# Kernel optimization log

Hardware: AMD Instinct MI355X
Metric: run time of the kernel (lower is better)

Reference implementation:

```python
import jax, jax.numpy as jnp
import numpy as np

B, T, N, IN, OUT = 8, 48, 512, 256, 256
GR, NR = 16, 8
ALPHA = 1.0


def setup_inputs() -> dict:
    key = jax.random.key(0)
    ks = jax.random.split(key, 6)
    scale = 1.0 / np.sqrt(IN)
    x = jax.random.normal(ks[0], (B, T, N, IN), dtype=jnp.float32)
    W = jax.random.uniform(ks[1], (OUT, IN), jnp.float32, -scale, scale)
    b = jnp.zeros((OUT,), jnp.float32)
    gA = jax.random.uniform(ks[2], (IN, GR), jnp.float32, -scale, scale)
    gB = jax.random.uniform(ks[3], (GR, OUT), jnp.float32, -scale, scale) * 0.1
    nA = jax.random.uniform(ks[4], (N, IN, NR), jnp.float32, -scale, scale)
    nB = jax.random.uniform(ks[5], (N, NR, OUT), jnp.float32, -scale, scale) * 0.1
    return {"x": x, "W": W, "b": b, "gA": gA, "gB": gB, "nA": nA, "nB": nB}


def reference(x, W, b, gA, gB, nA, nB):
    # dense base: x @ W.T + b
    base = jnp.einsum('btni,oi->btno', x, W) + b
    # global LoRA: (x @ gA) @ gB * alpha/global_rank
    g = jnp.einsum('btnr,ro->btno', jnp.einsum('btni,ir->btnr', x, gA), gB) * (ALPHA / GR)
    # per-node LoRA
    p1 = jnp.einsum('btni,nir->btnr', x, nA)
    nd = jnp.einsum('btnr,nro->btno', p1, nB) * (ALPHA / NR)
    return base + g + nd
```

## Files before the change

kernel.cpp:

```cpp
#include <hip/hip_runtime.h>


typedef __attribute__((ext_vector_type(4))) float f32x4;
typedef __attribute__((ext_vector_type(8))) short short8;

__device__ __forceinline__ unsigned short f2bf(float f) {
    unsigned int u = __builtin_bit_cast(unsigned int, f);
    u += 0x7fffu + ((u >> 16) & 1u);
    return (unsigned short)(u >> 16);
}

__device__ __forceinline__ short8 cvt8(f32x4 a, f32x4 b) {
    short8 r;
    r[0] = (short)f2bf(a[0]); r[1] = (short)f2bf(a[1]);
    r[2] = (short)f2bf(a[2]); r[3] = (short)f2bf(a[3]);
    r[4] = (short)f2bf(b[0]); r[5] = (short)f2bf(b[1]);
    r[6] = (short)f2bf(b[2]); r[7] = (short)f2bf(b[3]);
    return r;
}

__global__ __launch_bounds__(512, 1) void fused_node_lora(
    const float* __restrict__ x, const float* __restrict__ W,
    const float* __restrict__ bias, const float* __restrict__ gA,
    const float* __restrict__ gB, const float* __restrict__ nA,
    const float* __restrict__ nB, float* __restrict__ out)
{
    extern __shared__ __align__(16) char smem[];
    const int n    = blockIdx.x;
    const int tid  = threadIdx.x;
    const int lane = tid & 63;
    const int w    = tid >> 6;
    const int l15  = lane & 15;
    const int kblk = lane >> 4;

    {
        short8 afr[2];
        #pragma unroll
        for (int t = 0; t < 2; ++t) {
            const int i = (w * 2 + t) * 16 + l15;
            const float* ap = (kblk == 2) ? (nA + ((long)n * 256 + i) * 8)
                                          : (gA + (long)i * 16 + (kblk & 1) * 8);
            const float sc = (kblk == 2) ? 0.125f : ((kblk == 3) ? 0.0f : 0.0625f);
            const float4 q0 = *(const float4*)(ap);
            const float4 q1 = *(const float4*)(ap + 4);
            short8 a;
            a[0] = (short)f2bf(q0.x * sc); a[1] = (short)f2bf(q0.y * sc);
            a[2] = (short)f2bf(q0.z * sc); a[3] = (short)f2bf(q0.w * sc);
            a[4] = (short)f2bf(q1.x * sc); a[5] = (short)f2bf(q1.y * sc);
            a[6] = (short)f2bf(q1.z * sc); a[7] = (short)f2bf(q1.w * sc);
            afr[t] = a;
        }
        for (int ot = 0; ot < 16; ++ot) {
            const int o = ot * 16 + l15;
            const float* bp = (kblk == 0) ? (gB + o)
                             : (kblk == 1) ? (gB + 2048 + o)
                                           : (nB + (long)n * 2048 + o);
            short8 bfr;
            #pragma unroll
            for (int j = 0; j < 8; ++j) bfr[j] = (short)f2bf(bp[j * 256]);
            const f32x4 zero = {0.f, 0.f, 0.f, 0.f};
            f32x4 c0 = __builtin_amdgcn_mfma_f32_16x16x32_bf16(afr[0], bfr, zero, 0, 0, 0);
            f32x4 c1 = __builtin_amdgcn_mfma_f32_16x16x32_bf16(afr[1], bfr, zero, 0, 0, 0);
            #pragma unroll
            for (int t = 0; t < 2; ++t) {
                const f32x4 c = t ? c1 : c0;
                const int ib = (w * 2 + t) * 16 + kblk * 4;
                const float4 wv = *(const float4*)(W + (long)o * 256 + ib);
                unsigned int lo = (unsigned int)f2bf(wv.x + c[0]) |
                                  ((unsigned int)f2bf(wv.y + c[1]) << 16);
                unsigned int hi = (unsigned int)f2bf(wv.z + c[2]) |
                                  ((unsigned int)f2bf(wv.w + c[3]) << 16);
                int byte = (o << 9) + (ib << 1);
                byte ^= ((o & 7) << 4);
                *reinterpret_cast<uint2*>(smem + byte) = make_uint2(lo, hi);
            }
        }
    }
    __syncthreads();

    const float* xbase = x + ((long)(w * 16 + l15) * 512 + n) * 256 + kblk * 8;
    const long RSTR = 128L * 512 * 256;

    f32x4 pfa[3], pfb[3];
    #define LDX(t) do {                                                        \
        const f32x4* _p = (const f32x4*)(xbase + ((t) >> 3) * RSTR + ((t) & 7) * 32); \
        pfa[(t) % 3] = __builtin_nontemporal_load(_p);                         \
        pfb[(t) % 3] = __builtin_nontemporal_load(_p + 1);                     \
    } while (0)

    LDX(0); LDX(1); LDX(2);

    #pragma unroll
    for (int rtl = 0; rtl < 3; ++rtl) {
        f32x4 acc[16];
        #pragma unroll
        for (int ot = 0; ot < 16; ++ot) { const f32x4 z = {0.f,0.f,0.f,0.f}; acc[ot] = z; }

        #pragma unroll
        for (int kt = 0; kt < 8; ++kt) {
            const int t = rtl * 8 + kt;
            const short8 af = cvt8(pfa[t % 3], pfb[t % 3]);
            if (t + 3 < 24) LDX(t + 3);
            const unsigned int kaddr =
                ((((unsigned)l15 << 9) | ((unsigned)kt << 6) | ((unsigned)kblk << 4))
                 ^ (((unsigned)(l15 & 7)) << 4));
            #pragma unroll
            for (int ot = 0; ot < 16; ++ot) {
                const short8 bf = *reinterpret_cast<const short8*>(smem + kaddr + ot * 8192);
                acc[ot] = __builtin_amdgcn_mfma_f32_16x16x32_bf16(bf, af, acc[ot], 0, 0, 0);
            }
        }

        const int rt = w + rtl * 8;
        float* obase = out + ((long)(rt * 16 + l15) * 512 + n) * 256 + kblk * 4;
        #pragma unroll
        for (int ot = 0; ot < 16; ++ot) {
            const f32x4 bv = *(const f32x4*)(bias + ot * 16 + kblk * 4);
            f32x4 v = acc[ot];
            v[0] += bv[0]; v[1] += bv[1]; v[2] += bv[2]; v[3] += bv[3];
            __builtin_nontemporal_store(v, (f32x4*)(obase + ot * 16));
        }
    }
    #undef LDX
}

extern "C" void kernel_launch(void* const* d_in, const int* in_sizes, int n_in,
                              void* d_out, int out_size, void* d_ws, size_t ws_size,
                              hipStream_t stream) {
    const float* x  = (const float*)d_in[0];
    const float* W  = (const float*)d_in[1];
    const float* b  = (const float*)d_in[2];
    const float* gA = (const float*)d_in[3];
    const float* gB = (const float*)d_in[4];
    const float* nA = (const float*)d_in[5];
    const float* nB = (const float*)d_in[6];
    float* out = (float*)d_out;
    (void)hipFuncSetAttribute((const void*)fused_node_lora,
                              hipFuncAttributeMaxDynamicSharedMemorySize, 131072);
    fused_node_lora<<<dim3(512), dim3(512), 131072, stream>>>(x, W, b, gA, gB, nA, nB, out);
}
```

Before: 125.5 us.

## Split waves across output halves and reuse each LDS B fragment across three row tiles

The main GEMM loop is reorganised so each wave owns 8 of the 16 output column tiles and processes three 16-row x tiles at once, in two passes. Each LDS read of a weight fragment now feeds three MFMAs instead of one, which halves LDS traffic per MFMA. The cost is that each x row tile is loaded and converted by two waves instead of one. Register use also grows from three buffered x chunks to nine, and the loads switch from nontemporal to plain.

```diff
diff --git a/kernel.cpp b/kernel.cpp
--- a/kernel.cpp
+++ b/kernel.cpp
@@ -78,47 +78,63 @@
     }
     __syncthreads();
 
-    const float* xbase = x + ((long)(w * 16 + l15) * 512 + n) * 256 + kblk * 8;
-    const long RSTR = 128L * 512 * 256;
+    const int wm = w & 3;
+    const int wo = w >> 2;
+    const long TSTR = 16L * 512 * 256;
+    const float* xb = x + ((long)(wm * 96 + l15) * 512 + n) * 256 + kblk * 8;
 
-    f32x4 pfa[3], pfb[3];
-    #define LDX(t) do {                                                        \
-        const f32x4* _p = (const f32x4*)(xbase + ((t) >> 3) * RSTR + ((t) & 7) * 32); \
-        pfa[(t) % 3] = __builtin_nontemporal_load(_p);                         \
-        pfb[(t) % 3] = __builtin_nontemporal_load(_p + 1);                     \
-    } while (0)
+    f32x4 buf[3][3][2];
+    #define LDX(s2) do {                                                          \
+        const int _p = (s2) >> 3, _k = (s2) & 7;                                  \
+        _Pragma("unroll")                                                         \
+        for (int _j = 0; _j < 3; ++_j) {                                          \
+            const f32x4* _q = (const f32x4*)(xb + (long)(_p * 3 + _j) * TSTR + _k * 32); \
+            buf[(s2) % 3][_j][0] = _q[0];                                         \
+            buf[(s2) % 3][_j][1] = _q[1];                                         \
+        } } while (0)
 
     LDX(0); LDX(1); LDX(2);
 
     #pragma unroll
-    for (int rtl = 0; rtl < 3; ++rtl) {
-        f32x4 acc[16];
+    for (int p = 0; p < 2; ++p) {
+        f32x4 acc[3][8];
         #pragma unroll
-        for (int ot = 0; ot < 16; ++ot) { const f32x4 z = {0.f,0.f,0.f,0.f}; acc[ot] = z; }
+        for (int j = 0; j < 3; ++j)
+            #pragma unroll
+            for (int oi = 0; oi < 8; ++oi) { const f32x4 z = {0.f,0.f,0.f,0.f}; acc[j][oi] = z; }
 
         #pragma unroll
         for (int kt = 0; kt < 8; ++kt) {
-            const int t = rtl * 8 + kt;
-            const short8 af = cvt8(pfa[t % 3], pfb[t % 3]);
-            if (t + 3 < 24) LDX(t + 3);
+            const int s = p * 8 + kt;
+            short8 af[3];
+            #pragma unroll
+            for (int j = 0; j < 3; ++j) af[j] = cvt8(buf[s % 3][j][0], buf[s % 3][j][1]);
+            if (s + 3 < 16) LDX(s + 3);
             const unsigned int kaddr =
                 ((((unsigned)l15 << 9) | ((unsigned)kt << 6) | ((unsigned)kblk << 4))
                  ^ (((unsigned)(l15 & 7)) << 4));
             #pragma unroll
-            for (int ot = 0; ot < 16; ++ot) {
-                const short8 bf = *reinterpret_cast<const short8*>(smem + kaddr + ot * 8192);
-                acc[ot] = __builtin_amdgcn_mfma_f32_16x16x32_bf16(bf, af, acc[ot], 0, 0, 0);
+            for (int oi = 0; oi < 8; ++oi) {
+                const short8 bf = *reinterpret_cast<const short8*>(
+                    smem + kaddr + (unsigned)(wo * 8 + oi) * 8192u);
+                #pragma unroll
+                for (int j = 0; j < 3; ++j)
+                    acc[j][oi] = __builtin_amdgcn_mfma_f32_16x16x32_bf16(bf, af[j], acc[j][oi], 0, 0, 0);
             }
         }
 
-        const int rt = w + rtl * 8;
-        float* obase = out + ((long)(rt * 16 + l15) * 512 + n) * 256 + kblk * 4;
         #pragma unroll
-        for (int ot = 0; ot < 16; ++ot) {
+        for (int oi = 0; oi < 8; ++oi) {
+            const int ot = wo * 8 + oi;
             const f32x4 bv = *(const f32x4*)(bias + ot * 16 + kblk * 4);
-            f32x4 v = acc[ot];
-            v[0] += bv[0]; v[1] += bv[1]; v[2] += bv[2]; v[3] += bv[3];
-            __builtin_nontemporal_store(v, (f32x4*)(obase + ot * 16));
+            #pragma unroll
+            for (int j = 0; j < 3; ++j) {
+                f32x4 v = acc[j][oi];
+                v[0] += bv[0]; v[1] += bv[1]; v[2] += bv[2]; v[3] += bv[3];
+                float* ob = out + ((long)((wm * 6 + p * 3 + j) * 16 + l15) * 512 + n) * 256
+                            + ot * 16 + kblk * 4;
+                __builtin_nontemporal_store(v, (f32x4*)ob);
+            }
         }
     }
     #undef LDX
```

New measurement: 107.9 us. 1.16x faster.
